# Optimization experiments

Measured on AMD Instinct MI355X. Metric: run time of the kernel, lower is better.

The kernel has to match this reference:

```python
import jax, jax.numpy as jnp
import numpy as np

T_MAX = 201  # TEXT_MAX_LEN
HID = 512
VOCAB = 100  # NUM_CHAR
BATCH = 2048


def setup_inputs() -> dict:
    key = jax.random.key(0)
    ks = jax.random.split(key, 8)
    s = 0.05  # keep gates in a sane range
    return {
        "feat": jax.random.normal(ks[0], (BATCH, HID), jnp.float32),      # resnet pooler_output
        "W_ih": jax.random.normal(ks[1], (3 * HID, HID), jnp.float32) * s,  # torch weight_ih_l0 (r,z,n)
        "W_hh": jax.random.normal(ks[2], (3 * HID, HID), jnp.float32) * s,
        "b_ih": jax.random.normal(ks[3], (3 * HID,), jnp.float32) * s,
        "b_hh": jax.random.normal(ks[4], (3 * HID,), jnp.float32) * s,
        "W_proj": jax.random.normal(ks[5], (VOCAB, HID), jnp.float32) * s,
        "b_proj": jax.random.normal(ks[6], (VOCAB,), jnp.float32) * s,
        "embed": jax.random.normal(ks[7], (VOCAB, HID), jnp.float32) * s,
        "sos": 0,
    }


def _gru_cell(x, h, W_ih, W_hh, b_ih, b_hh):
    # torch GRU cell: gates ordered (reset, update, new)
    gi = x @ W_ih.T + b_ih            # [B, 3H]
    gh = h @ W_hh.T + b_hh            # [B, 3H]
    i_r, i_z, i_n = jnp.split(gi, 3, axis=-1)
    h_r, h_z, h_n = jnp.split(gh, 3, axis=-1)
    r = jax.nn.sigmoid(i_r + h_r)
    z = jax.nn.sigmoid(i_z + h_z)
    n = jnp.tanh(i_n + r * h_n)
    return (1.0 - z) * n + z * h


def reference(feat, W_ih, W_hh, b_ih, b_hh, W_proj, b_proj, embed, sos):
    B = feat.shape[0]
    # start token embedding broadcast over batch
    x0 = jnp.broadcast_to(embed[sos], (B, HID))
    h0 = feat  # encoder features initialize the GRU hidden state

    def step(carry, _):
        h, x = carry
        h = _gru_cell(x, h, W_ih, W_hh, b_ih, b_hh)
        logits = h @ W_proj.T + b_proj          # [B, V]
        pred = jnp.argmax(logits, axis=-1)      # greedy decode
        x_next = embed[pred]                    # [B, H]
        return (h, x_next), logits

    _, logits_tbv = jax.lax.scan(step, (h0, x0), None, length=T_MAX)  # [T, B, V]
    # outputs.permute(0, 2, 1): [B, V, T]
    return jnp.transpose(logits_tbv, (1, 2, 0))
```

## Files before the change

### kernel.cpp

```cpp
#include <hip/hip_runtime.h>
#include <cmath>

#define HID   512
#define VOCAB 100
#define G3    1536
#define GEXT  1664
#define NT    104
#define TMAX  201
#define ROWS  8
#define BLOCK 512
#define NWG   256
#define TPW   13

typedef __bf16 bf16x8 __attribute__((ext_vector_type(8)));
typedef float  f32x4  __attribute__((ext_vector_type(4)));

#define SZ_WPK   (NT * 16 * 2 * 64 * 8)
#define FBASE    (SZ_WPK / 2)
#define OFF_EIH  FBASE
#define SZ_EIH   (VOCAB * G3)
#define OFF_WIHT (OFF_EIH + SZ_EIH)
#define SZ_WIHT  (HID * G3)
#define OFF_BEXT (OFF_WIHT + SZ_WIHT)

__global__ void prep_kernel(const float* __restrict__ W_ih,
                            const float* __restrict__ b_hh,
                            const float* __restrict__ b_proj,
                            float* __restrict__ ws)
{
  int idx = blockIdx.x * 256 + threadIdx.x;
  if (idx < SZ_WIHT) {
    int k = idx / G3, j = idx - k * G3;
    ws[OFF_WIHT + idx] = W_ih[j * HID + k];
  } else if (idx < SZ_WIHT + GEXT) {
    int j = idx - SZ_WIHT;
    float v = 0.f;
    if (j < G3)              v = b_hh[j];
    else if (j < G3 + VOCAB) v = b_proj[j - G3];
    ws[OFF_BEXT + j] = v;
  }
}

__global__ void pack_kernel(const float* __restrict__ W_hh,
                            const float* __restrict__ W_proj,
                            __bf16* __restrict__ wpk)
{
  int idx = blockIdx.x * 256 + threadIdx.x;
  if (idx >= NT * 16 * 64 * 8) return;
  int j    = idx & 7;
  int lane = (idx >> 3) & 63;
  int ks   = (idx >> 9) & 15;
  int c    = idx >> 13;
  int col  = c * 16 + (lane & 15);
  int k    = ks * 32 + (lane >> 4) * 8 + j;
  float w = 0.f;
  if (col < G3)              w = W_hh[col * HID + k];
  else if (col < G3 + VOCAB) w = W_proj[(col - G3) * HID + k];
  __bf16 hi = (__bf16)w;
  __bf16 lo = (__bf16)(w - (float)hi);
  int base = (((c * 16 + ks) * 2) * 64 + lane) * 8 + j;
  wpk[base]       = hi;
  wpk[base + 512] = lo;
}

__global__ void eih_kernel(const float* __restrict__ embed,
                           const float* __restrict__ b_ih,
                           float* __restrict__ ws)
{
  int v = blockIdx.x / 6;
  int j = (blockIdx.x % 6) * 256 + threadIdx.x;
  const float* WihT = ws + OFF_WIHT;
  const float* e = embed + v * HID;
  float acc = b_ih[j];
  for (int k = 0; k < HID; ++k)
    acc = fmaf(WihT[k * G3 + j], e[k], acc);
  ws[OFF_EIH + v * G3 + j] = acc;
}

__global__ __launch_bounds__(BLOCK, 2) void decode_kernel(
    const float* __restrict__ feat,
    const int* __restrict__ sos,
    const float* __restrict__ ws,
    const __bf16* __restrict__ wpk,
    float* __restrict__ out)
{
  __shared__ __align__(16) char hab[16 * 1024];
  __shared__ float gh[ROWS][GEXT + 1];
  __shared__ int   pred_lds[ROWS];

  const float* __restrict__ EIH  = ws + OFF_EIH;
  const float* __restrict__ bext = ws + OFF_BEXT;

  const int tid  = threadIdx.x;
  const int lane = tid & 63;
  const int wv   = tid >> 6;
  const int b0   = blockIdx.x * ROWS;

  float h[ROWS];
  #pragma unroll
  for (int r = 0; r < ROWS; ++r) {
    float f = feat[(size_t)(b0 + r) * HID + tid];
    h[r] = f;
    __bf16 hi = (__bf16)f;
    __bf16 lo = (__bf16)(f - (float)hi);
    unsigned so = ((unsigned)(tid * 2)) ^ (((unsigned)(r & 7)) << 4);
    *(__bf16*)(hab + (r << 10) + so)       = hi;
    *(__bf16*)(hab + ((r + 8) << 10) + so) = lo;
  }
  if (tid < ROWS) pred_lds[tid] = sos[0];
  __syncthreads();

  const int      arow  = lane & 15;
  const unsigned abase = (unsigned)(arow << 10);
  const unsigned axor  = ((unsigned)(arow & 7)) << 4;
  const unsigned ag    = (unsigned)((lane >> 4) << 4);

  for (int t = 0; t <= TMAX; ++t) {
    bf16x8 afr[16];
    #pragma unroll
    for (int ks = 0; ks < 16; ++ks)
      afr[ks] = *(const bf16x8*)(hab + abase + ((((unsigned)ks << 6) + ag) ^ axor));

    for (int tt = 0; tt < TPW; ++tt) {
      int tile = wv * TPW + tt;
      f32x4 acc = {0.f, 0.f, 0.f, 0.f};
      const bf16x8* bp = ((const bf16x8*)wpk) + ((size_t)tile * 32 * 64 + lane);
      #pragma unroll
      for (int ks = 0; ks < 16; ++ks) {
        bf16x8 bh = bp[ks * 128];
        bf16x8 bl = bp[ks * 128 + 64];
        acc = __builtin_amdgcn_mfma_f32_16x16x32_bf16(afr[ks], bh, acc, 0, 0, 0);
        acc = __builtin_amdgcn_mfma_f32_16x16x32_bf16(afr[ks], bl, acc, 0, 0, 0);
      }
      int colw = tile * 16 + (lane & 15);
      float bias = bext[colw];
      float vsum[4];
      #pragma unroll
      for (int i = 0; i < 4; ++i)
        vsum[i] = acc[i] + __shfl_xor(acc[i], 32, 64);
      if (lane < 32) {
        int rbase = (lane >> 4) * 4;
        #pragma unroll
        for (int i = 0; i < 4; ++i)
          gh[rbase + i][colw] = vsum[i] + bias;
      }
    }
    __syncthreads();

    if (t >= 1) {
      if (tid < VOCAB) {
        #pragma unroll
        for (int r = 0; r < ROWS; ++r)
          __builtin_nontemporal_store(
              gh[r][G3 + tid],
              &out[((size_t)(b0 + r) * VOCAB + tid) * TMAX + (t - 1)]);
      }
      if (t < TMAX && tid < ROWS) {
        float best = gh[tid][G3];
        int bi = 0;
        for (int x = 1; x < VOCAB; ++x) {
          float val = gh[tid][G3 + x];
          if (val > best) { best = val; bi = x; }
        }
        pred_lds[tid] = bi;
      }
    }
    __syncthreads();

    if (t < TMAX) {
      const int u = tid;
      #pragma unroll
      for (int r = 0; r < ROWS; ++r) {
        const float* eb = EIH + (size_t)pred_lds[r] * G3;
        float rg = 1.f / (1.f + expf(-(eb[u]           + gh[r][u])));
        float zg = 1.f / (1.f + expf(-(eb[HID + u]     + gh[r][HID + u])));
        float ng = tanhf(eb[2 * HID + u] + rg * gh[r][2 * HID + u]);
        h[r] = (1.f - zg) * ng + zg * h[r];
        __bf16 hi = (__bf16)h[r];
        __bf16 lo = (__bf16)(h[r] - (float)hi);
        unsigned so = ((unsigned)(u * 2)) ^ (((unsigned)(r & 7)) << 4);
        *(__bf16*)(hab + (r << 10) + so)       = hi;
        *(__bf16*)(hab + ((r + 8) << 10) + so) = lo;
      }
    }
    __syncthreads();
  }
}

extern "C" void kernel_launch(void* const* d_in, const int* in_sizes, int n_in,
                              void* d_out, int out_size, void* d_ws, size_t ws_size,
                              hipStream_t stream)
{
  const float* feat   = (const float*)d_in[0];
  const float* W_ih   = (const float*)d_in[1];
  const float* W_hh   = (const float*)d_in[2];
  const float* b_ih   = (const float*)d_in[3];
  const float* b_hh   = (const float*)d_in[4];
  const float* W_proj = (const float*)d_in[5];
  const float* b_proj = (const float*)d_in[6];
  const float* embed  = (const float*)d_in[7];
  const int*   sos    = (const int*)d_in[8];

  float*  wsf = (float*)d_ws;
  __bf16* wpk = (__bf16*)d_ws;
  float*  out = (float*)d_out;

  const int prep_total = SZ_WIHT + GEXT;
  prep_kernel<<<(prep_total + 255) / 256, 256, 0, stream>>>(W_ih, b_hh, b_proj, wsf);
  pack_kernel<<<(NT * 16 * 64 * 8 + 255) / 256, 256, 0, stream>>>(W_hh, W_proj, wpk);
  eih_kernel<<<600, 256, 0, stream>>>(embed, b_ih, wsf);
  decode_kernel<<<NWG, BLOCK, 0, stream>>>(feat, sos, wsf, wpk, out);
}
```

Baseline: 7.294 ms.

## Process 16 batch rows per workgroup with separate hi/lo MFMA terms

Doubles rows per workgroup to 16 (1024 threads, 128 workgroups) so each streamed weight tile is reused across twice as many batch rows. The old layout packed hi/lo activations as 16 A-rows and summed halves by shuffle. Now hi and lo are separate A operands, giving four MFMAs per k-step (hi*hi, lo*hi, hi*lo, lo*lo). Argmax becomes a per-wave shuffle reduction, the final step skips gate tiles, and weight loads are nontemporal. The trade is more MFMA work and lower occupancy for half the global weight traffic per row.

```diff
diff --git a/kernel.cpp b/kernel.cpp
--- a/kernel.cpp
+++ b/kernel.cpp
@@ -7,10 +7,10 @@
 #define GEXT  1664
 #define NT    104
 #define TMAX  201
-#define ROWS  8
-#define BLOCK 512
-#define NWG   256
-#define TPW   13
+#define ROWS  16
+#define BLOCK 1024
+#define NWAVE 16
+#define NWG   128
 
 typedef __bf16 bf16x8 __attribute__((ext_vector_type(8)));
 typedef float  f32x4  __attribute__((ext_vector_type(4)));
@@ -77,14 +77,14 @@
   ws[OFF_EIH + v * G3 + j] = acc;
 }
 
-__global__ __launch_bounds__(BLOCK, 2) void decode_kernel(
+__global__ __launch_bounds__(BLOCK) void decode_kernel(
     const float* __restrict__ feat,
     const int* __restrict__ sos,
     const float* __restrict__ ws,
     const __bf16* __restrict__ wpk,
     float* __restrict__ out)
 {
-  __shared__ __align__(16) char hab[16 * 1024];
+  __shared__ __align__(16) char hab[32 * 1024];
   __shared__ float gh[ROWS][GEXT + 1];
   __shared__ int   pred_lds[ROWS];
 
@@ -95,92 +95,93 @@
   const int lane = tid & 63;
   const int wv   = tid >> 6;
   const int b0   = blockIdx.x * ROWS;
-
-  float h[ROWS];
+  const int u    = tid & (HID - 1);
+  const int rb   = (tid >> 9) * 8;
+
+  float h[8];
   #pragma unroll
-  for (int r = 0; r < ROWS; ++r) {
-    float f = feat[(size_t)(b0 + r) * HID + tid];
-    h[r] = f;
+  for (int r8 = 0; r8 < 8; ++r8) {
+    int r = rb + r8;
+    float f = feat[(size_t)(b0 + r) * HID + u];
+    h[r8] = f;
     __bf16 hi = (__bf16)f;
     __bf16 lo = (__bf16)(f - (float)hi);
-    unsigned so = ((unsigned)(tid * 2)) ^ (((unsigned)(r & 7)) << 4);
-    *(__bf16*)(hab + (r << 10) + so)       = hi;
-    *(__bf16*)(hab + ((r + 8) << 10) + so) = lo;
+    unsigned so = ((unsigned)(u * 2)) ^ (((unsigned)(r & 7)) << 4);
+    *(__bf16*)(hab + (r << 10) + so)        = hi;
+    *(__bf16*)(hab + ((r + 16) << 10) + so) = lo;
   }
   if (tid < ROWS) pred_lds[tid] = sos[0];
   __syncthreads();
 
-  const int      arow  = lane & 15;
-  const unsigned abase = (unsigned)(arow << 10);
-  const unsigned axor  = ((unsigned)(arow & 7)) << 4;
-  const unsigned ag    = (unsigned)((lane >> 4) << 4);
+  const int      arow = lane & 15;
+  const unsigned ag   = (unsigned)((lane >> 4) << 4);
+  const unsigned axor = ((unsigned)(arow & 7)) << 4;
+  const char* ha_hi = hab + (arow << 10);
+  const char* ha_lo = ha_hi + (16 << 10);
 
   for (int t = 0; t <= TMAX; ++t) {
-    bf16x8 afr[16];
-    #pragma unroll
-    for (int ks = 0; ks < 16; ++ks)
-      afr[ks] = *(const bf16x8*)(hab + abase + ((((unsigned)ks << 6) + ag) ^ axor));
-
-    for (int tt = 0; tt < TPW; ++tt) {
-      int tile = wv * TPW + tt;
+    for (int tile = wv; tile < NT; tile += NWAVE) {
+      if (t == TMAX && tile < 96) continue;
       f32x4 acc = {0.f, 0.f, 0.f, 0.f};
-      const bf16x8* bp = ((const bf16x8*)wpk) + ((size_t)tile * 32 * 64 + lane);
-      #pragma unroll
+      const bf16x8* bp = ((const bf16x8*)wpk) + (size_t)tile * 2048 + lane;
+      #pragma unroll 4
       for (int ks = 0; ks < 16; ++ks) {
-        bf16x8 bh = bp[ks * 128];
-        bf16x8 bl = bp[ks * 128 + 64];
-        acc = __builtin_amdgcn_mfma_f32_16x16x32_bf16(afr[ks], bh, acc, 0, 0, 0);
-        acc = __builtin_amdgcn_mfma_f32_16x16x32_bf16(afr[ks], bl, acc, 0, 0, 0);
+        unsigned aoff = (((unsigned)ks << 6) + ag) ^ axor;
+        bf16x8 ahi = *(const bf16x8*)(ha_hi + aoff);
+        bf16x8 alo = *(const bf16x8*)(ha_lo + aoff);
+        bf16x8 bhi = __builtin_nontemporal_load(bp + ks * 128);
+        bf16x8 blo = __builtin_nontemporal_load(bp + ks * 128 + 64);
+        acc = __builtin_amdgcn_mfma_f32_16x16x32_bf16(ahi, bhi, acc, 0, 0, 0);
+        acc = __builtin_amdgcn_mfma_f32_16x16x32_bf16(alo, bhi, acc, 0, 0, 0);
+        acc = __builtin_amdgcn_mfma_f32_16x16x32_bf16(ahi, blo, acc, 0, 0, 0);
+        acc = __builtin_amdgcn_mfma_f32_16x16x32_bf16(alo, blo, acc, 0, 0, 0);
       }
       int colw = tile * 16 + (lane & 15);
       float bias = bext[colw];
-      float vsum[4];
+      int r0 = (lane >> 4) * 4;
       #pragma unroll
       for (int i = 0; i < 4; ++i)
-        vsum[i] = acc[i] + __shfl_xor(acc[i], 32, 64);
-      if (lane < 32) {
-        int rbase = (lane >> 4) * 4;
-        #pragma unroll
-        for (int i = 0; i < 4; ++i)
-          gh[rbase + i][colw] = vsum[i] + bias;
-      }
+        gh[r0 + i][colw] = acc[i] + bias;
     }
     __syncthreads();
 
     if (t >= 1) {
-      if (tid < VOCAB) {
+      for (int i = tid; i < ROWS * VOCAB; i += BLOCK) {
+        int r = i / VOCAB, v = i - r * VOCAB;
+        __builtin_nontemporal_store(
+            gh[r][G3 + v],
+            &out[((size_t)(b0 + r) * VOCAB + v) * TMAX + (t - 1)]);
+      }
+      if (t < TMAX) {
+        float v0 = (lane < VOCAB)      ? gh[wv][G3 + lane]      : -1e30f;
+        float v1 = (lane + 64 < VOCAB) ? gh[wv][G3 + 64 + lane] : -1e30f;
+        float bv; int bi;
+        if (v0 >= v1) { bv = v0; bi = lane; } else { bv = v1; bi = lane + 64; }
         #pragma unroll
-        for (int r = 0; r < ROWS; ++r)
-          __builtin_nontemporal_store(
-              gh[r][G3 + tid],
-              &out[((size_t)(b0 + r) * VOCAB + tid) * TMAX + (t - 1)]);
-      }
-      if (t < TMAX && tid < ROWS) {
-        float best = gh[tid][G3];
-        int bi = 0;
-        for (int x = 1; x < VOCAB; ++x) {
-          float val = gh[tid][G3 + x];
-          if (val > best) { best = val; bi = x; }
+        for (int off = 32; off >= 1; off >>= 1) {
+          float ov = __shfl_xor(bv, off);
+          int   oi = __shfl_xor(bi, off);
+          if (ov > bv || (ov == bv && oi < bi)) { bv = ov; bi = oi; }
         }
-        pred_lds[tid] = bi;
+        if (lane == 0) pred_lds[wv] = bi;
       }
     }
     __syncthreads();
 
     if (t < TMAX) {
-      const int u = tid;
       #pragma unroll
-      for (int r = 0; r < ROWS; ++r) {
+      for (int r8 = 0; r8 < 8; ++r8) {
+        int r = rb + r8;
         const float* eb = EIH + (size_t)pred_lds[r] * G3;
         float rg = 1.f / (1.f + expf(-(eb[u]           + gh[r][u])));
         float zg = 1.f / (1.f + expf(-(eb[HID + u]     + gh[r][HID + u])));
         float ng = tanhf(eb[2 * HID + u] + rg * gh[r][2 * HID + u]);
-        h[r] = (1.f - zg) * ng + zg * h[r];
-        __bf16 hi = (__bf16)h[r];
-        __bf16 lo = (__bf16)(h[r] - (float)hi);
+        h[r8] = (1.f - zg) * ng + zg * h[r8];
+        __bf16 hi = (__bf16)h[r8];
+        __bf16 lo = (__bf16)(h[r8] - (float)hi);
         unsigned so = ((unsigned)(u * 2)) ^ (((unsigned)(r & 7)) << 4);
-        *(__bf16*)(hab + (r << 10) + so)       = hi;
-        *(__bf16*)(hab + ((r + 8) << 10) + so) = lo;
+        *(__bf16*)(hab + (r << 10) + so)        = hi;
+        *(__bf16*)(hab + ((r + 16) << 10) + so) = lo;
       }
     }
     __syncthreads();
```

Result: slower. 13.46 ms (+84.5%).
